# Kernel tuning notes

Measured on AMD Instinct MI355X. Metric: run time of the kernel, lower is better.

## Reference

```python
import jax, jax.numpy as jnp
import numpy as np

N = 100000
E = 1600000
F_IN = 256
H1, C1 = 8, 8          # conv1: 8 heads x 8 channels -> 64
H2, C2 = 1, 32         # conv2: 1 head x num_classes
SLOPE = 0.2


def gat_conv(x, src, dst, n, W, a_src, a_dst, b, heads, out):
    # x: [n, f_in]; W: [f_in, heads*out]; a_src/a_dst: [heads, out]; b: [heads*out]
    h = (x @ W).reshape(n, heads, out)                       # [n, H, C]
    s = jnp.sum(h * a_src, axis=-1)                          # [n, H]
    d = jnp.sum(h * a_dst, axis=-1)                          # [n, H]
    e = jax.nn.leaky_relu(s[src] + d[dst], SLOPE)            # [e, H]
    m = jax.ops.segment_max(e, dst, num_segments=n)          # stable segment softmax
    ex = jnp.exp(e - m[dst])
    z = jax.ops.segment_sum(ex, dst, num_segments=n)
    alpha = ex / (z[dst] + 1e-16)                            # [e, H]
    msg = alpha[:, :, None] * h[src]                         # [e, H, C]
    agg = jax.ops.segment_sum(msg, dst, num_segments=n)      # [n, H, C]
    return agg.reshape(n, heads * out) + b


def setup_inputs() -> dict:
    key = jax.random.key(0)
    ks = jax.random.split(key, 10)
    x = jax.random.normal(ks[0], (N, F_IN), dtype=jnp.float32)
    edge_index = jax.random.randint(ks[1], (2, E), 0, N, dtype=jnp.int32)
    sc = 0.05
    W1 = jax.random.normal(ks[2], (F_IN, H1 * C1), dtype=jnp.float32) * sc
    att_src1 = jax.random.normal(ks[3], (H1, C1), dtype=jnp.float32) * sc
    att_dst1 = jax.random.normal(ks[4], (H1, C1), dtype=jnp.float32) * sc
    b1 = jnp.zeros((H1 * C1,), dtype=jnp.float32)
    W2 = jax.random.normal(ks[5], (H1 * C1, H2 * C2), dtype=jnp.float32) * sc
    att_src2 = jax.random.normal(ks[6], (H2, C2), dtype=jnp.float32) * sc
    att_dst2 = jax.random.normal(ks[7], (H2, C2), dtype=jnp.float32) * sc
    b2 = jnp.zeros((H2 * C2,), dtype=jnp.float32)
    return {"x": x, "edge_index": edge_index, "W1": W1, "att_src1": att_src1,
            "att_dst1": att_dst1, "b1": b1, "W2": W2, "att_src2": att_src2,
            "att_dst2": att_dst2, "b2": b2}


def reference(x, edge_index, W1, att_src1, att_dst1, b1, W2, att_src2, att_dst2, b2):
    # add self loops (PyG GATConv default)
    loops = jnp.arange(N, dtype=edge_index.dtype)
    src = jnp.concatenate([edge_index[0], loops])
    dst = jnp.concatenate([edge_index[1], loops])
    # dropout layers are identity in eval mode
    h = gat_conv(x, src, dst, N, W1, att_src1, att_dst1, b1, H1, C1)
    h = jax.nn.elu(h)
    h = gat_conv(h, src, dst, N, W2, att_src2, att_dst2, b2, H2, C2)
    return jax.nn.log_softmax(h, axis=1)
```

## Files before the change

### kernel.cpp

```cpp
#include <hip/hip_runtime.h>
#include <hip/hip_bf16.h>

#define N_NODES 100000
#define N_EDGES 1600000
#define N_TOT   (N_EDGES + N_NODES)
#define F_IN    256
#define F1      64
#define H1      8
#define C1      8
#define F2      32
#define SLOPE   0.2f
#define CHUNK   2048
#define NCH     ((N_NODES + CHUNK - 1) / CHUNK)

#define NB_G    ((N_NODES + 255) / 256)
#define NB_H    ((N_EDGES + 255) / 256)

#define SLICES  8
#define SL_W    ((N_NODES + SLICES - 1) / SLICES)
#define CH_E    16384
#define NCHUNK  ((N_EDGES + CH_E - 1) / CH_E)

typedef unsigned int  uint;
typedef unsigned short ushort;
typedef __attribute__((ext_vector_type(8))) short bf16x8;
typedef __attribute__((ext_vector_type(4))) float f32x4;

__device__ inline ushort f2bf(float f) {
    uint u = __float_as_uint(f);
    uint r = u + 0x7fffu + ((u >> 16) & 1u);
    return (ushort)(r >> 16);
}
__device__ inline float bflo(uint u) { return __uint_as_float(u << 16); }
__device__ inline float bfhi(uint u) { return __uint_as_float(u & 0xffff0000u); }
__device__ inline uint pk2bf(float a, float b) {
    __hip_bfloat162 h = __float22bfloat162_rn(make_float2(a, b));
    union { __hip_bfloat162 h; uint u; } cv; cv.h = h;
    return cv.u;
}

__global__ __launch_bounds__(256) void k_gemm1_hist(
        const float* __restrict__ x, const float* __restrict__ W1,
        const float* __restrict__ as1, const float* __restrict__ ad1,
        const int* __restrict__ ei,
        ushort* __restrict__ h1b, float* __restrict__ s1, float* __restrict__ d1,
        int* __restrict__ cnt, int* __restrict__ rank) {
    __shared__ union {
        ushort B[F_IN * F1];
        ushort S[4][64][66];
    } sm;
    const int tid = threadIdx.x;

    if (blockIdx.x >= NB_G) {
        const int e = (blockIdx.x - NB_G) * 256 + tid;
        if (e < N_EDGES)
            rank[e] = atomicAdd(cnt + ei[N_EDGES + e], 1);
        return;
    }

    for (int i = 0; i < 64; ++i) {
        const int e = i * 256 + tid;
        const int k = e >> 6, n = e & 63;
        sm.B[((k >> 3) * 64 + n) * 8 + (k & 7)] = f2bf(W1[e]);
    }
    __syncthreads();

    const int wave = tid >> 6, lane = tid & 63;
    const int q = lane >> 4, ln = lane & 15;
    const int rowbase = blockIdx.x * 256 + wave * 64;

    f32x4 acc[4][4];
#pragma unroll
    for (int mt = 0; mt < 4; ++mt)
#pragma unroll
        for (int nt = 0; nt < 4; ++nt) acc[mt][nt] = (f32x4){0.f, 0.f, 0.f, 0.f};

    int rows[4];
#pragma unroll
    for (int mt = 0; mt < 4; ++mt) {
        const int r = rowbase + mt * 16 + ln;
        rows[mt] = r < N_NODES ? r : N_NODES - 1;
    }

    for (int t = 0; t < 8; ++t) {
        bf16x8 bfr[4];
#pragma unroll
        for (int nt = 0; nt < 4; ++nt)
            bfr[nt] = *(const bf16x8*)&sm.B[((t * 4 + q) * 64 + nt * 16 + ln) * 8];
#pragma unroll
        for (int mt = 0; mt < 4; ++mt) {
            const float4* ap = (const float4*)(x + (size_t)rows[mt] * F_IN + t * 32 + q * 8);
            const float4 a0 = ap[0], a1 = ap[1];
            uint4 au = make_uint4(pk2bf(a0.x, a0.y), pk2bf(a0.z, a0.w),
                                  pk2bf(a1.x, a1.y), pk2bf(a1.z, a1.w));
            bf16x8 af = *(bf16x8*)&au;
#pragma unroll
            for (int nt = 0; nt < 4; ++nt)
                acc[mt][nt] = __builtin_amdgcn_mfma_f32_16x16x32_bf16(
                                  af, bfr[nt], acc[mt][nt], 0, 0, 0);
        }
    }
    __syncthreads();

#pragma unroll
    for (int mt = 0; mt < 4; ++mt)
#pragma unroll
        for (int nt = 0; nt < 4; ++nt)
#pragma unroll
            for (int r = 0; r < 4; ++r)
                sm.S[wave][mt * 16 + q * 4 + r][nt * 16 + ln] = f2bf(acc[mt][nt][r]);
    __syncthreads();

    const int node = rowbase + lane;
    if (node >= N_NODES) return;
    const uint* srow = (const uint*)&sm.S[wave][lane][0];
    float sacc[H1], dacc[H1];
#pragma unroll
    for (int h = 0; h < H1; ++h) { sacc[h] = 0.f; dacc[h] = 0.f; }
    uint4* hout = (uint4*)(h1b + (size_t)node * F1);
#pragma unroll
    for (int p4 = 0; p4 < 8; ++p4) {
        const uint u0 = srow[p4 * 4 + 0], u1 = srow[p4 * 4 + 1];
        const uint u2 = srow[p4 * 4 + 2], u3 = srow[p4 * 4 + 3];
        hout[p4] = make_uint4(u0, u1, u2, u3);
        const float c[8] = {bflo(u0), bfhi(u0), bflo(u1), bfhi(u1),
                            bflo(u2), bfhi(u2), bflo(u3), bfhi(u3)};
#pragma unroll
        for (int j = 0; j < 8; ++j) {
            sacc[p4] += c[j] * as1[p4 * 8 + j];
            dacc[p4] += c[j] * ad1[p4 * 8 + j];
        }
    }
    float4* s4 = (float4*)(s1 + (size_t)node * H1);
    float4* d4 = (float4*)(d1 + (size_t)node * H1);
    s4[0] = make_float4(sacc[0], sacc[1], sacc[2], sacc[3]);
    s4[1] = make_float4(sacc[4], sacc[5], sacc[6], sacc[7]);
    d4[0] = make_float4(dacc[0], dacc[1], dacc[2], dacc[3]);
    d4[1] = make_float4(dacc[4], dacc[5], dacc[6], dacc[7]);
}

__global__ __launch_bounds__(256) void k_scan_a(
        const int* __restrict__ cnt, int* __restrict__ row_ptr,
        int* __restrict__ bsum) {
    __shared__ int sdata[256];
    const int tid = threadIdx.x;
    const int base = blockIdx.x * CHUNK + tid * 8;
    int v[8];
    int tot = 0;
#pragma unroll
    for (int j = 0; j < 8; ++j) {
        v[j] = (base + j < N_NODES) ? cnt[base + j] + 1 : 0;
        tot += v[j];
    }
    sdata[tid] = tot;
    __syncthreads();
    for (int off = 1; off < 256; off <<= 1) {
        int t = (tid >= off) ? sdata[tid - off] : 0;
        __syncthreads();
        sdata[tid] += t;
        __syncthreads();
    }
    int run = sdata[tid] - tot;
#pragma unroll
    for (int j = 0; j < 8; ++j) {
        if (base + j < N_NODES) row_ptr[base + j] = run;
        run += v[j];
    }
    if (tid == 255) bsum[blockIdx.x] = sdata[255];
}

__global__ __launch_bounds__(256) void k_scan_c2(
        int* __restrict__ row_ptr, const int* __restrict__ bsum,
        int* __restrict__ srcs) {
    __shared__ int pb[64];
    const int t = threadIdx.x;
    if (t < 64) {
        int v = (t < NCH) ? bsum[t] : 0;
        const int orig = v;
        for (int off = 1; off < 64; off <<= 1) {
            int u = __shfl_up(v, off);
            if (t >= off) v += u;
        }
        pb[t] = v - orig;
    }
    __syncthreads();
    const int i = blockIdx.x * 256 + t;
    if (i < N_NODES) {
        const int rp = row_ptr[i] + pb[i / CHUNK];
        row_ptr[i] = rp;
        srcs[rp] = i;
    } else if (i == N_NODES) row_ptr[N_NODES] = N_TOT;
}

__global__ __launch_bounds__(256) void k_scatter(
        const int* __restrict__ ei, const int* __restrict__ row_ptr,
        const int* __restrict__ rank, int* __restrict__ srcs) {
    const int slice = blockIdx.x % SLICES;
    const int chunk = blockIdx.x / SLICES;
    const int lo = slice * SL_W;
    const int base = chunk * CH_E;
    const int lim = (base + CH_E < N_EDGES) ? base + CH_E : N_EDGES;
    for (int i = base + threadIdx.x; i < lim; i += 256) {
        const int di = ei[N_EDGES + i];
        if ((uint)(di - lo) < (uint)SL_W)
            srcs[row_ptr[di] + 1 + rank[i]] = ei[i];
    }
}

__global__ __launch_bounds__(256) void k_agg1(
        const int* __restrict__ row_ptr, const int* __restrict__ srcs,
        const ushort* __restrict__ h1b, const float* __restrict__ s1,
        const float* __restrict__ d1, const float* __restrict__ b1,
        const float* __restrict__ W2, const float* __restrict__ as2,
        const float* __restrict__ ad2,
        ushort* __restrict__ h2b, float* __restrict__ s2,
        float* __restrict__ d2) {
    __shared__ float sx[4][64];
    const int wid = (blockIdx.x * 256 + threadIdx.x) >> 6;
    if (wid >= N_NODES) return;
    const int w = threadIdx.x >> 6;
    const int lane = threadIdx.x & 63;
    const int q = lane >> 3;
    const int c = lane & 7;
    const float dh = d1[(size_t)wid * H1 + c];
    const int beg = row_ptr[wid], end = row_ptr[wid + 1];
    const uint4* hv = (const uint4*)h1b;
    float a0 = 0.f, a1 = 0.f, a2 = 0.f, a3 = 0.f;
    float a4 = 0.f, a5 = 0.f, a6 = 0.f, a7 = 0.f, z = 0.f;
    int i = beg + q;
    for (; i + 8 < end; i += 16) {
        const int sA = srcs[i], sB = srcs[i + 8];
        float eA = s1[(size_t)sA * H1 + c] + dh;
        float eB = s1[(size_t)sB * H1 + c] + dh;
        eA = eA > 0.f ? eA : SLOPE * eA;
        eB = eB > 0.f ? eB : SLOPE * eB;
        const float xA = __expf(eA), xB = __expf(eB);
        const uint4 UA = hv[(size_t)sA * 8 + c];
        const uint4 UB = hv[(size_t)sB * 8 + c];
        z  += xA + xB;
        a0 += xA * bflo(UA.x) + xB * bflo(UB.x);
        a1 += xA * bfhi(UA.x) + xB * bfhi(UB.x);
        a2 += xA * bflo(UA.y) + xB * bflo(UB.y);
        a3 += xA * bfhi(UA.y) + xB * bfhi(UB.y);
        a4 += xA * bflo(UA.z) + xB * bflo(UB.z);
        a5 += xA * bfhi(UA.z) + xB * bfhi(UB.z);
        a6 += xA * bflo(UA.w) + xB * bflo(UB.w);
        a7 += xA * bfhi(UA.w) + xB * bfhi(UB.w);
    }
    for (; i < end; i += 8) {
        const int sA = srcs[i];
        float eA = s1[(size_t)sA * H1 + c] + dh;
        eA = eA > 0.f ? eA : SLOPE * eA;
        const float xA = __expf(eA);
        const uint4 UA = hv[(size_t)sA * 8 + c];
        z  += xA;
        a0 += xA * bflo(UA.x);
        a1 += xA * bfhi(UA.x);
        a2 += xA * bflo(UA.y);
        a3 += xA * bfhi(UA.y);
        a4 += xA * bflo(UA.z);
        a5 += xA * bfhi(UA.z);
        a6 += xA * bflo(UA.w);
        a7 += xA * bfhi(UA.w);
    }
#pragma unroll
    for (int off = 8; off <= 32; off <<= 1) {
        a0 += __shfl_xor(a0, off); a1 += __shfl_xor(a1, off);
        a2 += __shfl_xor(a2, off); a3 += __shfl_xor(a3, off);
        a4 += __shfl_xor(a4, off); a5 += __shfl_xor(a5, off);
        a6 += __shfl_xor(a6, off); a7 += __shfl_xor(a7, off);
        z  += __shfl_xor(z, off);
    }
    if (lane < 8) {
        const float zi = 1.f / (z + 1e-16f);
        float v0 = a0 * zi + b1[c * 8 + 0];
        float v1 = a1 * zi + b1[c * 8 + 1];
        float v2 = a2 * zi + b1[c * 8 + 2];
        float v3 = a3 * zi + b1[c * 8 + 3];
        float v4 = a4 * zi + b1[c * 8 + 4];
        float v5 = a5 * zi + b1[c * 8 + 5];
        float v6 = a6 * zi + b1[c * 8 + 6];
        float v7 = a7 * zi + b1[c * 8 + 7];
        v0 = v0 > 0.f ? v0 : __expf(v0) - 1.f;
        v1 = v1 > 0.f ? v1 : __expf(v1) - 1.f;
        v2 = v2 > 0.f ? v2 : __expf(v2) - 1.f;
        v3 = v3 > 0.f ? v3 : __expf(v3) - 1.f;
        v4 = v4 > 0.f ? v4 : __expf(v4) - 1.f;
        v5 = v5 > 0.f ? v5 : __expf(v5) - 1.f;
        v6 = v6 > 0.f ? v6 : __expf(v6) - 1.f;
        v7 = v7 > 0.f ? v7 : __expf(v7) - 1.f;
        *(float4*)&sx[w][c * 8 + 0] = make_float4(v0, v1, v2, v3);
        *(float4*)&sx[w][c * 8 + 4] = make_float4(v4, v5, v6, v7);
    }
    __builtin_amdgcn_wave_barrier();

    const int kh = lane >> 5;
    const int oc = lane & 31;
    const float4* sxv = (const float4*)&sx[w][kh * 32];
    const float* wp0 = W2 + (size_t)(kh * 32) * F2 + oc;
    float acc = 0.f;
#pragma unroll
    for (int k4 = 0; k4 < 8; ++k4) {
        const float4 xv = sxv[k4];
        const float* wp = wp0 + (size_t)k4 * 4 * F2;
        acc += xv.x * wp[0]      + xv.y * wp[F2]
             + xv.z * wp[2 * F2] + xv.w * wp[3 * F2];
    }
    acc += __shfl_xor(acc, 32);

    float sA2 = acc * as2[oc], dA2 = acc * ad2[oc];
#pragma unroll
    for (int off = 1; off <= 16; off <<= 1) {
        sA2 += __shfl_xor(sA2, off);
        dA2 += __shfl_xor(dA2, off);
    }
    if (lane < 32) h2b[(size_t)wid * F2 + oc] = f2bf(acc);
    if (lane == 0) { s2[wid] = sA2; d2[wid] = dA2; }
}

__global__ __launch_bounds__(256) void k_agg2(
        const int* __restrict__ row_ptr, const int* __restrict__ srcs,
        const ushort* __restrict__ h2b, const float* __restrict__ s2,
        const float* __restrict__ d2, const float* __restrict__ b2,
        float* __restrict__ out) {
    const int wid = (blockIdx.x * 256 + threadIdx.x) >> 6;
    if (wid >= N_NODES) return;
    const int lane = threadIdx.x & 63;
    const int q = lane >> 2;
    const int c = lane & 3;
    const float dn = d2[wid];
    const int beg = row_ptr[wid], end = row_ptr[wid + 1];
    const uint4* hv = (const uint4*)h2b;
    float a0 = 0.f, a1 = 0.f, a2 = 0.f, a3 = 0.f;
    float a4 = 0.f, a5 = 0.f, a6 = 0.f, a7 = 0.f, z = 0.f;
    int i = beg + q;
    for (; i + 16 < end; i += 32) {
        const int sA = srcs[i], sB = srcs[i + 16];
        float eA = s2[sA] + dn;
        float eB = s2[sB] + dn;
        eA = eA > 0.f ? eA : SLOPE * eA;
        eB = eB > 0.f ? eB : SLOPE * eB;
        const float xA = __expf(eA), xB = __expf(eB);
        const uint4 UA = hv[(size_t)sA * 4 + c];
        const uint4 UB = hv[(size_t)sB * 4 + c];
        z  += xA + xB;
        a0 += xA * bflo(UA.x) + xB * bflo(UB.x);
        a1 += xA * bfhi(UA.x) + xB * bfhi(UB.x);
        a2 += xA * bflo(UA.y) + xB * bflo(UB.y);
        a3 += xA * bfhi(UA.y) + xB * bfhi(UB.y);
        a4 += xA * bflo(UA.z) + xB * bflo(UB.z);
        a5 += xA * bfhi(UA.z) + xB * bfhi(UB.z);
        a6 += xA * bflo(UA.w) + xB * bflo(UB.w);
        a7 += xA * bfhi(UA.w) + xB * bfhi(UB.w);
    }
    for (; i < end; i += 16) {
        const int sA = srcs[i];
        float eA = s2[sA] + dn;
        eA = eA > 0.f ? eA : SLOPE * eA;
        const float xA = __expf(eA);
        const uint4 UA = hv[(size_t)sA * 4 + c];
        z  += xA;
        a0 += xA * bflo(UA.x);
        a1 += xA * bfhi(UA.x);
        a2 += xA * bflo(UA.y);
        a3 += xA * bfhi(UA.y);
        a4 += xA * bflo(UA.z);
        a5 += xA * bfhi(UA.z);
        a6 += xA * bflo(UA.w);
        a7 += xA * bfhi(UA.w);
    }
#pragma unroll
    for (int off = 4; off <= 32; off <<= 1) {
        a0 += __shfl_xor(a0, off); a1 += __shfl_xor(a1, off);
        a2 += __shfl_xor(a2, off); a3 += __shfl_xor(a3, off);
        a4 += __shfl_xor(a4, off); a5 += __shfl_xor(a5, off);
        a6 += __shfl_xor(a6, off); a7 += __shfl_xor(a7, off);
        z  += __shfl_xor(z, off);
    }
    const float zi = 1.f / (z + 1e-16f);
    const float v0 = a0 * zi + b2[8 * c + 0];
    const float v1 = a1 * zi + b2[8 * c + 1];
    const float v2 = a2 * zi + b2[8 * c + 2];
    const float v3 = a3 * zi + b2[8 * c + 3];
    const float v4 = a4 * zi + b2[8 * c + 4];
    const float v5 = a5 * zi + b2[8 * c + 5];
    const float v6 = a6 * zi + b2[8 * c + 6];
    const float v7 = a7 * zi + b2[8 * c + 7];
    float m = fmaxf(fmaxf(fmaxf(v0, v1), fmaxf(v2, v3)),
                    fmaxf(fmaxf(v4, v5), fmaxf(v6, v7)));
#pragma unroll
    for (int off = 1; off <= 2; off <<= 1) m = fmaxf(m, __shfl_xor(m, off));
    float ssum = __expf(v0 - m) + __expf(v1 - m) + __expf(v2 - m) + __expf(v3 - m)
               + __expf(v4 - m) + __expf(v5 - m) + __expf(v6 - m) + __expf(v7 - m);
#pragma unroll
    for (int off = 1; off <= 2; off <<= 1) ssum += __shfl_xor(ssum, off);
    const float lse = m + __logf(ssum);
    if (lane < 4) {
        float4* o4 = (float4*)out;
        o4[(size_t)wid * 8 + 2 * c + 0] =
            make_float4(v0 - lse, v1 - lse, v2 - lse, v3 - lse);
        o4[(size_t)wid * 8 + 2 * c + 1] =
            make_float4(v4 - lse, v5 - lse, v6 - lse, v7 - lse);
    }
}

extern "C" void kernel_launch(void* const* d_in, const int* in_sizes, int n_in,
                              void* d_out, int out_size, void* d_ws, size_t ws_size,
                              hipStream_t stream) {
    const float* x   = (const float*)d_in[0];
    const int*   ei  = (const int*)d_in[1];
    const float* W1  = (const float*)d_in[2];
    const float* as1 = (const float*)d_in[3];
    const float* ad1 = (const float*)d_in[4];
    const float* b1  = (const float*)d_in[5];
    const float* W2  = (const float*)d_in[6];
    const float* as2 = (const float*)d_in[7];
    const float* ad2 = (const float*)d_in[8];
    const float* b2  = (const float*)d_in[9];
    float* out = (float*)d_out;

    ushort* h1b = (ushort*)d_ws;
    ushort* h2b = h1b + (size_t)N_NODES * F1;
    float*  s1  = (float*)(h2b + (size_t)N_NODES * F2);
    float*  d1  = s1 + (size_t)N_NODES * H1;
    float*  s2  = d1 + (size_t)N_NODES * H1;
    float*  d2  = s2 + N_NODES;
    int* cnt     = (int*)(d2 + N_NODES);
    int* rank    = cnt + N_NODES;
    int* row_ptr = rank + N_EDGES;
    int* bsum    = row_ptr + N_NODES + 1;
    int* srcs    = bsum + 64;

    hipMemsetAsync(cnt, 0, (size_t)N_NODES * sizeof(int), stream);

    const int nb_w = (N_NODES * 64 + 255) / 256;

    k_gemm1_hist<<<NB_G + NB_H, 256, 0, stream>>>(x, W1, as1, ad1, ei,
                                                  h1b, s1, d1, cnt, rank);
    k_scan_a<<<NCH, 256, 0, stream>>>(cnt, row_ptr, bsum);
    k_scan_c2<<<(N_NODES + 256) / 256, 256, 0, stream>>>(row_ptr, bsum, srcs);
    k_scatter<<<SLICES * NCHUNK, 256, 0, stream>>>(ei, row_ptr, rank, srcs);
    k_agg1<<<nb_w, 256, 0, stream>>>(row_ptr, srcs, h1b, s1, d1, b1,
                                     W2, as2, ad2, h2b, s2, d2);
    k_agg2<<<nb_w, 256, 0, stream>>>(row_ptr, srcs, h2b, s2, d2, b2, out);
}
```

Baseline: 397.7 us.

## Replace global-atomic CSR build with two-level bucketed counting sort

Builds the destination-sorted CSR with a radix-style bucketed counting sort instead of per-edge global atomics plus a sliced scatter. Edges are first histogrammed per block into 256-node buckets in shared memory, then column-scanned and scattered as (src,dst) pairs into a bucket-ordered temp buffer. Per-bucket kernels then compute node counts and final positions using LDS atomics only. The aim is to remove contended global atomics and the eightfold re-reading of edges in the old scatter. The cost is extra kernel launches, a temp pair buffer and more passes over the edge data, and edge order within a node becomes nondeterministic.

```diff
diff --git a/kernel.cpp b/kernel.cpp
--- a/kernel.cpp
+++ b/kernel.cpp
@@ -14,12 +14,11 @@
 #define NCH     ((N_NODES + CHUNK - 1) / CHUNK)
 
 #define NB_G    ((N_NODES + 255) / 256)
-#define NB_H    ((N_EDGES + 255) / 256)
-
-#define SLICES  8
-#define SL_W    ((N_NODES + SLICES - 1) / SLICES)
-#define CH_E    16384
-#define NCHUNK  ((N_EDGES + CH_E - 1) / CH_E)
+
+#define EB      4096
+#define NB1     ((N_EDGES + EB - 1) / EB)
+#define BW      256
+#define NBKT    ((N_NODES + BW - 1) / BW)
 
 typedef unsigned int  uint;
 typedef unsigned short ushort;
@@ -39,22 +38,49 @@
     return cv.u;
 }
 
-__global__ __launch_bounds__(256) void k_gemm1_hist(
+__device__ inline void bucket_bases(const int* __restrict__ colsum,
+                                    int* sc, int* sb, int tid) {
+    const int i0 = 2 * tid, i1 = 2 * tid + 1;
+    const int a0 = (i0 < NBKT) ? colsum[i0] : 0;
+    const int a1 = (i1 < NBKT) ? colsum[i1] : 0;
+    sc[tid] = a0 + a1;
+    __syncthreads();
+    for (int off = 1; off < 256; off <<= 1) {
+        int t = (tid >= off) ? sc[tid - off] : 0;
+        __syncthreads();
+        sc[tid] += t;
+        __syncthreads();
+    }
+    const int excl = sc[tid] - (a0 + a1);
+    if (i0 < NBKT)  sb[i0] = excl;
+    if (i1 <= NBKT) sb[i1] = excl + a0;
+    __syncthreads();
+}
+
+__global__ __launch_bounds__(256) void k_gemm1_p1(
         const float* __restrict__ x, const float* __restrict__ W1,
         const float* __restrict__ as1, const float* __restrict__ ad1,
         const int* __restrict__ ei,
         ushort* __restrict__ h1b, float* __restrict__ s1, float* __restrict__ d1,
-        int* __restrict__ cnt, int* __restrict__ rank) {
+        int* __restrict__ bcnt) {
     __shared__ union {
         ushort B[F_IN * F1];
         ushort S[4][64][66];
+        int    H[NBKT];
     } sm;
     const int tid = threadIdx.x;
 
     if (blockIdx.x >= NB_G) {
-        const int e = (blockIdx.x - NB_G) * 256 + tid;
-        if (e < N_EDGES)
-            rank[e] = atomicAdd(cnt + ei[N_EDGES + e], 1);
+        const int blk = blockIdx.x - NB_G;
+        for (int j = tid; j < NBKT; j += 256) sm.H[j] = 0;
+        __syncthreads();
+        const int e0 = blk * EB;
+        const int lim = (e0 + EB < N_EDGES) ? e0 + EB : N_EDGES;
+        for (int i = e0 + tid; i < lim; i += 256)
+            atomicAdd(&sm.H[ei[N_EDGES + i] >> 8], 1);
+        __syncthreads();
+        for (int j = tid; j < NBKT; j += 256)
+            bcnt[j * NB1 + blk] = sm.H[j];
         return;
     }
 
@@ -137,6 +163,61 @@
     s4[1] = make_float4(sacc[4], sacc[5], sacc[6], sacc[7]);
     d4[0] = make_float4(dacc[0], dacc[1], dacc[2], dacc[3]);
     d4[1] = make_float4(dacc[4], dacc[5], dacc[6], dacc[7]);
+}
+
+__global__ __launch_bounds__(64) void k_p2(
+        int* __restrict__ bcnt, int* __restrict__ colsum) {
+    const int col = blockIdx.x, lane = threadIdx.x;
+    int carry = 0;
+    for (int c0 = 0; c0 < NB1; c0 += 64) {
+        const int idx = c0 + lane;
+        const int v = (idx < NB1) ? bcnt[col * NB1 + idx] : 0;
+        int s = v;
+#pragma unroll
+        for (int off = 1; off < 64; off <<= 1) {
+            int u = __shfl_up(s, off);
+            if (lane >= off) s += u;
+        }
+        if (idx < NB1) bcnt[col * NB1 + idx] = carry + s - v;
+        carry += __shfl(s, 63);
+    }
+    if (lane == 0) colsum[col] = carry;
+}
+
+__global__ __launch_bounds__(256) void k_p3(
+        const int* __restrict__ ei, const int* __restrict__ bcnt,
+        const int* __restrict__ colsum, int2* __restrict__ tmp) {
+    __shared__ int sc[256];
+    __shared__ int cur[NBKT + 1];
+    const int tid = threadIdx.x, blk = blockIdx.x;
+    bucket_bases(colsum, sc, cur, tid);
+    for (int b = tid; b < NBKT; b += 256) cur[b] += bcnt[b * NB1 + blk];
+    __syncthreads();
+    const int e0 = blk * EB;
+    const int lim = (e0 + EB < N_EDGES) ? e0 + EB : N_EDGES;
+    for (int i = e0 + tid; i < lim; i += 256) {
+        const int s = ei[i], d = ei[N_EDGES + i];
+        const int pos = atomicAdd(&cur[d >> 8], 1);
+        tmp[pos] = make_int2(s, d);
+    }
+}
+
+__global__ __launch_bounds__(256) void k_p4(
+        const int2* __restrict__ tmp, const int* __restrict__ colsum,
+        int* __restrict__ cnt) {
+    __shared__ int sc[256];
+    __shared__ int sb[NBKT + 1];
+    __shared__ int h[BW];
+    const int tid = threadIdx.x, b = blockIdx.x;
+    bucket_bases(colsum, sc, sb, tid);
+    h[tid] = 0;
+    __syncthreads();
+    const int lo = sb[b], hi = sb[b + 1];
+    for (int i = lo + tid; i < hi; i += 256)
+        atomicAdd(&h[tmp[i].y & (BW - 1)], 1);
+    __syncthreads();
+    const int n = b * BW + tid;
+    if (n < N_NODES) cnt[n] = h[tid];
 }
 
 __global__ __launch_bounds__(256) void k_scan_a(
@@ -192,18 +273,25 @@
     } else if (i == N_NODES) row_ptr[N_NODES] = N_TOT;
 }
 
-__global__ __launch_bounds__(256) void k_scatter(
-        const int* __restrict__ ei, const int* __restrict__ row_ptr,
-        const int* __restrict__ rank, int* __restrict__ srcs) {
-    const int slice = blockIdx.x % SLICES;
-    const int chunk = blockIdx.x / SLICES;
-    const int lo = slice * SL_W;
-    const int base = chunk * CH_E;
-    const int lim = (base + CH_E < N_EDGES) ? base + CH_E : N_EDGES;
-    for (int i = base + threadIdx.x; i < lim; i += 256) {
-        const int di = ei[N_EDGES + i];
-        if ((uint)(di - lo) < (uint)SL_W)
-            srcs[row_ptr[di] + 1 + rank[i]] = ei[i];
+__global__ __launch_bounds__(256) void k_p6(
+        const int2* __restrict__ tmp, const int* __restrict__ colsum,
+        const int* __restrict__ row_ptr, int* __restrict__ srcs) {
+    __shared__ int sc[256];
+    __shared__ int sb[NBKT + 1];
+    __shared__ int rp[BW];
+    __shared__ int cur[BW];
+    const int tid = threadIdx.x, b = blockIdx.x;
+    bucket_bases(colsum, sc, sb, tid);
+    const int n = b * BW + tid;
+    rp[tid] = (n < N_NODES) ? row_ptr[n] : 0;
+    cur[tid] = 0;
+    __syncthreads();
+    const int lo = sb[b], hi = sb[b + 1];
+    for (int i = lo + tid; i < hi; i += 256) {
+        const int2 e = tmp[i];
+        const int loc = e.y & (BW - 1);
+        const int r = atomicAdd(&cur[loc], 1);
+        srcs[rp[loc] + 1 + r] = e.x;
     }
 }
 
@@ -425,21 +513,24 @@
     float*  d1  = s1 + (size_t)N_NODES * H1;
     float*  s2  = d1 + (size_t)N_NODES * H1;
     float*  d2  = s2 + N_NODES;
-    int* cnt     = (int*)(d2 + N_NODES);
-    int* rank    = cnt + N_NODES;
-    int* row_ptr = rank + N_EDGES;
+    int2*   tmp = (int2*)(d2 + N_NODES);
+    int* cnt     = (int*)(tmp + N_EDGES);
+    int* row_ptr = cnt + N_NODES;
     int* bsum    = row_ptr + N_NODES + 1;
-    int* srcs    = bsum + 64;
-
-    hipMemsetAsync(cnt, 0, (size_t)N_NODES * sizeof(int), stream);
+    int* colsum  = bsum + 64;
+    int* bcnt    = colsum + NBKT;
+    int* srcs    = bcnt + (size_t)NBKT * NB1;
 
     const int nb_w = (N_NODES * 64 + 255) / 256;
 
-    k_gemm1_hist<<<NB_G + NB_H, 256, 0, stream>>>(x, W1, as1, ad1, ei,
-                                                  h1b, s1, d1, cnt, rank);
+    k_gemm1_p1<<<NB_G + NB1, 256, 0, stream>>>(x, W1, as1, ad1, ei,
+                                               h1b, s1, d1, bcnt);
+    k_p2<<<NBKT, 64, 0, stream>>>(bcnt, colsum);
+    k_p3<<<NB1, 256, 0, stream>>>(ei, bcnt, colsum, tmp);
+    k_p4<<<NBKT, 256, 0, stream>>>(tmp, colsum, cnt);
     k_scan_a<<<NCH, 256, 0, stream>>>(cnt, row_ptr, bsum);
     k_scan_c2<<<(N_NODES + 256) / 256, 256, 0, stream>>>(row_ptr, bsum, srcs);
-    k_scatter<<<SLICES * NCHUNK, 256, 0, stream>>>(ei, row_ptr, rank, srcs);
+    k_p6<<<NBKT, 256, 0, stream>>>(tmp, colsum, row_ptr, srcs);
     k_agg1<<<nb_w, 256, 0, stream>>>(row_ptr, srcs, h1b, s1, d1, b1,
                                      W2, as2, ad2, h2b, s2, d2);
     k_agg2<<<nb_w, 256, 0, stream>>>(row_ptr, srcs, h2b, s2, d2, b2, out);
```

After: 368.8 us. 1.08x faster.
